# Optimization experiments

Measured on AMD Instinct MI355X. Metric: run time of the kernel, lower is better.

Reference implementation:

```python
import jax, jax.numpy as jnp
import numpy as np
import math

B, H, L = 8, 512, 4096
N2 = 32  # d_state // 2


def setup_inputs() -> dict:
    key = jax.random.key(0)
    ks = jax.random.split(key, 8)
    u = jax.random.normal(ks[0], (B, H, L), dtype=jnp.float32)
    C = jax.random.normal(ks[1], (H, N2, 2), dtype=jnp.float32)  # view_as_real of cfloat C
    # log_dt ~ Uniform[log(dt_min), log(dt_max)], dt_min=1e-3, dt_max=0.1
    log_dt = jax.random.uniform(ks[2], (H,), dtype=jnp.float32,
                                minval=math.log(0.001), maxval=math.log(0.1))
    log_A_real = jnp.log(0.5 * jnp.ones((H, N2), dtype=jnp.float32))
    A_imag = math.pi * jnp.broadcast_to(jnp.arange(N2, dtype=jnp.float32), (H, N2))
    D = jax.random.normal(ks[3], (H,), dtype=jnp.float32)
    # pointwise Conv1d(H, 2H, kernel_size=1): weight (2H, H), bias (2H)
    fan = 1.0 / math.sqrt(H)
    W = jax.random.uniform(ks[4], (2 * H, H), dtype=jnp.float32, minval=-fan, maxval=fan)
    b = jax.random.uniform(ks[5], (2 * H,), dtype=jnp.float32, minval=-fan, maxval=fan)
    return {"u": u, "C": C, "log_dt": log_dt, "log_A_real": log_A_real,
            "A_imag": A_imag, "D": D, "W": W, "b": b}


def reference(u, C, log_dt, log_A_real, A_imag, D, W, b):
    Lb = u.shape[-1]
    # --- S4DKernel: kernel k of shape (H, L) ---
    dt = jnp.exp(log_dt)                                  # (H,)
    Cc = C[..., 0] + 1j * C[..., 1]                       # (H, N2) complex
    A = -jnp.exp(log_A_real) + 1j * A_imag                # (H, N2)
    dtA = A * dt[:, None]                                 # (H, N2)
    # Vandermonde: exp(dtA * l) for l in [0, L)
    K = jnp.exp(dtA[:, :, None] * jnp.arange(Lb, dtype=jnp.float32))  # (H, N2, L)
    Cmod = Cc * (jnp.exp(dtA) - 1.0) / A                  # (H, N2)
    k = 2.0 * jnp.einsum('hn,hnl->hl', Cmod, K).real      # (H, L)
    # --- FFT convolution (length 2L, causal) ---
    n = 2 * Lb
    k_f = jnp.fft.rfft(k, n=n)                            # (H, L+1)
    u_f = jnp.fft.rfft(u, n=n)                            # (B, H, L+1)
    y = jnp.fft.irfft(u_f * k_f, n=n)[..., :Lb]           # (B, H, L)
    # skip connection
    y = y + u * D[:, None]
    # activation (torch nn.GELU default = exact erf form)
    y = jax.nn.gelu(y, approximate=False)
    # pointwise conv (H -> 2H) + GLU over channel dim
    y = jnp.einsum('oh,bhl->bol', W, y) + b[None, :, None]  # (B, 2H, L)
    a, g = jnp.split(y, 2, axis=1)
    return a * jax.nn.sigmoid(g)                          # (B, H, L)
```

## Files before the change

kernel.cpp:

```cpp
#include <hip/hip_runtime.h>
#include <hip/hip_bf16.h>

constexpr int Bn = 8, Hn = 512, Ln = 4096, N2n = 32;

typedef _Float16 f16;
typedef __attribute__((ext_vector_type(8))) _Float16 f16x8;
typedef __attribute__((ext_vector_type(4))) _Float16 f16x4;
typedef __attribute__((ext_vector_type(2))) _Float16 f16x2;
typedef __attribute__((ext_vector_type(4))) float f32x4;

typedef void __attribute__((address_space(1))) gvoid;
typedef void __attribute__((address_space(3))) lvoid;

__global__ __launch_bounds__(64) void k_mats1(
    const float* __restrict__ C, const float* __restrict__ log_dt,
    const float* __restrict__ logA, const float* __restrict__ Aim,
    f16* __restrict__ Vg, f16* __restrict__ A3g, float2* __restrict__ w64g) {
  __shared__ f16 VT[64 * 64];
  __shared__ f16 QT[64 * 64];
  __shared__ float kp[64][33];
  __shared__ float ks[64];
  const int h = blockIdx.x, tid = threadIdx.x, n = tid & 31;

  if (tid < 32) {
    const int idx = h * N2n + n;
    float dt = expf(log_dt[h]);
    float Ar = -expf(logA[idx]);
    float Ai = Aim[idx];
    float dr = Ar * dt, di = Ai * dt;
    float er = expf(dr);
    float wr = er * cosf(di), wi = er * sinf(di);
    float den = Ar * Ar + Ai * Ai;
    float e1r = wr - 1.0f, e1i = wi;
    float tr = (e1r * Ar + e1i * Ai) / den;
    float ti = (e1i * Ar - e1r * Ai) / den;
    float Cr = C[idx * 2 + 0], Ci = C[idx * 2 + 1];
    float c2r = 2.0f * (Cr * tr - Ci * ti);
    float c2i = 2.0f * (Cr * ti + Ci * tr);

    float wpr = 1.f, wpi = 0.f;
    for (int p = 0; p <= 64; ++p) {
      float cwr = c2r * wpr - c2i * wpi;
      float cwi = c2r * wpi + c2i * wpr;
      if (p < 64) {
        const int j = 63 - p, ch = j >> 3, jo = j & 7;
        const int s0 = 2 * n, s1 = 2 * n + 1;
        VT[s0 * 64 + ((ch ^ (s0 & 7)) * 8) + jo] = (f16)wpr;
        VT[s1 * 64 + ((ch ^ (s1 & 7)) * 8) + jo] = (f16)wpi;
        kp[p][n] = cwr;
      }
      if (p >= 1) {
        const int t = p - 1, c0 = 2 * n;
        const int ch = (c0 >> 3) ^ (t & 7);
        QT[t * 64 + ch * 8 + (c0 & 7)]     = (f16)cwr;
        QT[t * 64 + ch * 8 + (c0 & 7) + 1] = (f16)(-cwi);
      }
      if (p == 64) w64g[h * 32 + n] = make_float2(wpr, wpi);
      float nr = wpr * wr - wpi * wi;
      float ni = wpr * wi + wpi * wr;
      wpr = nr; wpi = ni;
    }
  }
  __syncthreads();
  float s = 0.f;
#pragma unroll
  for (int m = 0; m < 32; ++m) s += kp[tid][m];
  ks[tid] = s;
  __syncthreads();
  const int t = tid;
#pragma unroll
  for (int c = 0; c < 8; ++c) {
    f16x8 row;
#pragma unroll
    for (int jo = 0; jo < 8; ++jo) {
      int j = c * 8 + jo;
      row[jo] = (j <= t) ? (f16)ks[t - j] : (f16)0.f;
    }
    *(f16x8*)&A3g[(size_t)h * 8192 + t * 128 + ((c ^ (t & 7)) * 8)] = row;
  }
#pragma unroll
  for (int c = 0; c < 8; ++c)
    *(f16x8*)&Vg[(size_t)h * 4096 + tid * 64 + c * 8] = *(f16x8*)&VT[tid * 64 + c * 8];
#pragma unroll
  for (int c = 0; c < 8; ++c)
    *(f16x8*)&A3g[(size_t)h * 8192 + tid * 128 + 64 + c * 8] = *(f16x8*)&QT[tid * 64 + c * 8];
}

__global__ void conv_w(const float* __restrict__ W, f16* __restrict__ Wh) {
  int i = blockIdx.x * 256 + threadIdx.x;
  if (i < 2 * Hn * Hn) Wh[i] = (f16)W[i];
}

__global__ __launch_bounds__(256, 4) void s4d_mid(
    const float* __restrict__ u, const f16* __restrict__ Vg,
    const f16* __restrict__ A3g, const float2* __restrict__ w64g,
    const float* __restrict__ Dv, f16* __restrict__ yg) {
  __shared__ f16 MATS[8192];
  __shared__ f16 U[4096];
  __shared__ f16 LE[4096];
  __shared__ float2 Pbuf[4][32];
  const int tid = threadIdx.x, wid = tid >> 6, lane = tid & 63;
  const int h = ((blockIdx.x >> 6) << 3) | (blockIdx.x & 7);
  const int b = (blockIdx.x >> 3) & 7;
  const float Dh = Dv[h];

#pragma unroll
  for (int q = 0; q < 2; ++q)
    __builtin_amdgcn_global_load_lds((const gvoid*)(Vg + (size_t)h * 4096 + (q * 256 + tid) * 8),
                                     (lvoid*)&MATS[(q * 256 + wid * 64) * 8], 16, 0, 0);
#pragma unroll
  for (int i = 0; i < 4; ++i) {
    int e = (i * 256 + tid) * 4;
    float4 uv = *(const float4*)(u + ((size_t)(b * Hn + h)) * Ln + e);
    int col = e >> 6, j = e & 63;
    f16x4 hv = {(f16)uv.x, (f16)uv.y, (f16)uv.z, (f16)uv.w};
    *(f16x4*)&U[col * 64 + ((j >> 3) ^ (col & 7)) * 8 + (j & 7)] = hv;
  }
  asm volatile("s_waitcnt vmcnt(0)" ::: "memory");
  __syncthreads();

  const int col = wid * 16 + (lane & 15);
  f32x4 acc[4];
#pragma unroll
  for (int i = 0; i < 4; ++i) acc[i] = (f32x4){0.f, 0.f, 0.f, 0.f};
#pragma unroll
  for (int ks = 0; ks < 2; ++ks) {
    const int kc = ks * 4 + (lane >> 4);
    f16x8 bv = *(const f16x8*)&U[col * 64 + ((kc ^ (col & 7)) * 8)];
#pragma unroll
    for (int mf = 0; mf < 4; ++mf) {
      int row = mf * 16 + (lane & 15);
      f16x8 a = *(const f16x8*)&MATS[row * 64 + ((kc ^ (row & 7)) * 8)];
      acc[mf] = __builtin_amdgcn_mfma_f32_16x16x32_f16(a, bv, acc[mf], 0, 0, 0);
    }
  }
  __syncthreads();

#pragma unroll
  for (int q = 0; q < 4; ++q)
    __builtin_amdgcn_global_load_lds((const gvoid*)(A3g + (size_t)h * 8192 + (q * 256 + tid) * 8),
                                     (lvoid*)&MATS[(q * 256 + wid * 64) * 8], 16, 0, 0);

#pragma unroll
  for (int mf = 0; mf < 4; ++mf) {
    int st0 = mf * 16 + (lane >> 4) * 4;
    f16x4 o = {(f16)acc[mf][0], (f16)acc[mf][1], (f16)acc[mf][2], (f16)acc[mf][3]};
    *(f16x4*)&LE[col * 64 + (((st0 >> 3) ^ (col & 7)) << 3) + (st0 & 7)] = o;
  }
  __syncthreads();

  {
    const int n = lane & 31, q = wid;
    const float2 wT = w64g[h * 32 + n];
    float qr = wT.x, qi = wT.y;
#pragma unroll
    for (int s = 0; s < 4; ++s) {
      float nr = qr * qr - qi * qi;
      float ni = 2.f * qr * qi;
      qr = nr; qi = ni;
    }
    f16x2 Lb[16];
    float er = 0.f, ei = 0.f;
    if (lane < 32) {
#pragma unroll
      for (int k = 0; k < 16; ++k) {
        int blk = q * 16 + k;
        int fi = blk * 64 + (((n >> 2) ^ (blk & 7)) << 3) + ((n & 3) << 1);
        Lb[k] = *(const f16x2*)&LE[fi];
      }
#pragma unroll
      for (int k = 0; k < 16; ++k) {
        float nr = fmaf(wT.x, er, fmaf(-wT.y, ei, (float)Lb[k][0]));
        float ni = fmaf(wT.y, er, fmaf(wT.x, ei, (float)Lb[k][1]));
        er = nr; ei = ni;
      }
      Pbuf[q][n] = make_float2(er, ei);
    }
    __syncthreads();
    if (lane < 32) {
      float orr = 0.f, oii = 0.f;
      for (int p = 0; p < q; ++p) {
        float2 Pp = Pbuf[p][n];
        float nr = fmaf(qr, orr, fmaf(-qi, oii, Pp.x));
        float ni = fmaf(qi, orr, fmaf(qr, oii, Pp.y));
        orr = nr; oii = ni;
      }
      er = orr; ei = oii;
#pragma unroll
      for (int k = 0; k < 16; ++k) {
        int blk = q * 16 + k;
        int fi = blk * 64 + (((n >> 2) ^ (blk & 7)) << 3) + ((n & 3) << 1);
        *(f16x2*)&LE[fi] = (f16x2){(f16)er, (f16)ei};
        float nr = fmaf(wT.x, er, fmaf(-wT.y, ei, (float)Lb[k][0]));
        float ni = fmaf(wT.y, er, fmaf(wT.x, ei, (float)Lb[k][1]));
        er = nr; ei = ni;
      }
    }
  }
  asm volatile("s_waitcnt vmcnt(0)" ::: "memory");
  __syncthreads();

  f32x4 acc4[4];
#pragma unroll
  for (int i = 0; i < 4; ++i) acc4[i] = (f32x4){0.f, 0.f, 0.f, 0.f};
#pragma unroll
  for (int ks = 0; ks < 4; ++ks) {
    const int kc = ks * 4 + (lane >> 4);
    f16x8 bf;
    if (ks < 2) bf = *(const f16x8*)&U[col * 64 + ((kc ^ (col & 7)) << 3)];
    else        bf = *(const f16x8*)&LE[col * 64 + (((kc - 8) ^ (col & 7)) << 3)];
#pragma unroll
    for (int mf = 0; mf < 4; ++mf) {
      int row = mf * 16 + (lane & 15);
      f16x8 af = *(const f16x8*)&MATS[row * 128 + ((kc ^ (row & 7)) << 3)];
      acc4[mf] = __builtin_amdgcn_mfma_f32_16x16x32_f16(af, bf, acc4[mf], 0, 0, 0);
    }
  }
  const int t0 = (lane >> 4) * 4;
#pragma unroll
  for (int mf = 0; mf < 4; ++mf) {
    const int tb = mf * 16 + t0;
    f16x4 uq = *(const f16x4*)&U[col * 64 + (((tb >> 3) ^ (col & 7)) << 3) + (tb & 7)];
    f16x4 o;
#pragma unroll
    for (int r = 0; r < 4; ++r) {
      float v = acc4[mf][r] + Dh * (float)uq[r];
      float g2 = v * fmaf(0.0713548163f, v * v, 1.5957691216f);
      o[r] = (f16)(v * __builtin_amdgcn_rcpf(1.0f + __expf(-g2)));
    }
    *(f16x4*)&yg[((size_t)(b * Hn + h)) * Ln + col * 64 + tb] = o;
  }
}

__global__ __launch_bounds__(256) void k_transpose(
    const f16* __restrict__ yg, f16* __restrict__ gyT) {
  __shared__ float T[64][65];
  const int bid = blockIdx.x, tid = threadIdx.x;
  const int b = bid >> 9, hg = (bid >> 6) & 7, lg = bid & 63;
  const int h0 = hg * 64, l0 = lg * 64;
  const int hi = tid >> 2, lc = (tid & 3) * 16;
  const f16* src = yg + ((size_t)(b * Hn + h0 + hi)) * Ln + l0 + lc;
  f16x8 v0 = *(const f16x8*)src;
  f16x8 v1 = *(const f16x8*)(src + 8);
#pragma unroll
  for (int e = 0; e < 8; ++e) T[lc + e][hi] = (float)v0[e];
#pragma unroll
  for (int e = 0; e < 8; ++e) T[lc + 8 + e][hi] = (float)v1[e];
  __syncthreads();
  const int li = tid >> 2, hc = (tid & 3) * 16;
  f16x8 o0, o1;
#pragma unroll
  for (int e = 0; e < 8; ++e) o0[e] = (f16)T[li][hc + e];
#pragma unroll
  for (int e = 0; e < 8; ++e) o1[e] = (f16)T[li][hc + 8 + e];
  f16* dst = gyT + ((size_t)b * Ln + l0 + li) * Hn + h0 + hc;
  *(f16x8*)dst = o0;
  *(f16x8*)(dst + 8) = o1;
}

__global__ __launch_bounds__(256, 3) void s4d_gemm(
    const f16* __restrict__ Wh, const f16* __restrict__ gyT,
    const float* __restrict__ bias, float* __restrict__ out) {
  __shared__ f16 As[2][2][64][32];
  __shared__ f16 Bs[2][128][32];
  __shared__ float biasS[2][64];
  const int tid = threadIdx.x;
  const int wid = tid >> 6, lane = tid & 63;
  const int nt = blockIdx.x & 255;
  const int mt = blockIdx.x >> 8;
  const int b = nt >> 5;
  const int l0 = (nt & 31) * 128;
  const int m0 = mt * 64;
  const int isG = wid >> 1;
  const int wn = wid & 1;

  if (tid < 64) biasS[0][tid] = bias[m0 + tid];
  else if (tid < 128) biasS[1][tid - 64] = bias[Hn + m0 + (tid - 64)];

  const int srow = lane >> 2;
  const int sp = lane & 3;

#define S4(r) ((((r) & 3)) ^ (((r) >> 2) & 3))

#define STAGE(BUF, KT)                                                                    \
  {                                                                                       \
    const int k0 = (KT) * 32;                                                             \
    _Pragma("unroll")                                                                     \
    for (int q = 0; q < 2; ++q) {                                                         \
      const int g = wid * 2 + q;                                                \
      const int ag = g >> 2, rq = g & 3;                                                  \
      const int r = rq * 16 + srow;                                                       \
      const f16* srcA = Wh + ((size_t)(ag * Hn + m0 + r) * 512 + k0 + ((sp ^ S4(r)) * 8)); \
      __builtin_amdgcn_global_load_lds((const gvoid*)srcA,                                \
          (lvoid*)&As[BUF][ag][rq * 16][0], 16, 0, 0);                                    \
    }                                                                                     \
    _Pragma("unroll")                                                                     \
    for (int q = 0; q < 2; ++q) {                                                         \
      const int rb = wid * 2 + q;                                               \
      const int r = rb * 16 + srow;                                                       \
      const f16* srcB = gyT + (((size_t)b * Ln + l0 + r) * Hn + k0 + ((sp ^ S4(r)) * 8)); \
      __builtin_amdgcn_global_load_lds((const gvoid*)srcB,                                \
          (lvoid*)&Bs[BUF][rb * 16][0], 16, 0, 0);                                        \
    }                                                                                     \
  }

  f32x4 acc[4][4];
#pragma unroll
  for (int i = 0; i < 4; ++i)
#pragma unroll
    for (int j = 0; j < 4; ++j) acc[i][j] = (f32x4){0.f, 0.f, 0.f, 0.f};

  STAGE(0, 0);
  asm volatile("s_waitcnt vmcnt(0)" ::: "memory");
  __syncthreads();

  const int kc = lane >> 4;
  for (int t = 0; t < 16; ++t) {
    const int cur = t & 1;
    if (t < 15) STAGE(cur ^ 1, t + 1);
    f16x8 af[4], bf[4];
#pragma unroll
    for (int mf = 0; mf < 4; ++mf) {
      const int row = mf * 16 + (lane & 15);
      af[mf] = *(const f16x8*)&As[cur][isG][row][(kc ^ S4(row)) * 8];
    }
#pragma unroll
    for (int nf = 0; nf < 4; ++nf) {
      const int cl = wn * 64 + nf * 16 + (lane & 15);
      bf[nf] = *(const f16x8*)&Bs[cur][cl][(kc ^ S4(cl)) * 8];
    }
#pragma unroll
    for (int mf = 0; mf < 4; ++mf)
#pragma unroll
      for (int nf = 0; nf < 4; ++nf)
        acc[mf][nf] = __builtin_amdgcn_mfma_f32_16x16x32_f16(af[mf], bf[nf], acc[mf][nf], 0, 0, 0);
    __syncthreads();
  }

  f16 (*SIG)[64][64] = (f16(*)[64][64]) & Bs[0][0][0];
  const int r0 = (lane >> 4) * 4, c0 = lane & 15;
  if (isG) {
#pragma unroll
    for (int mf = 0; mf < 4; ++mf) {
#pragma unroll
      for (int nf = 0; nf < 4; ++nf) {
#pragma unroll
        for (int r = 0; r < 4; ++r) {
          const int row = mf * 16 + r0 + r;
          float gv = acc[mf][nf][r] + biasS[1][row];
          SIG[wn][row][nf * 16 + c0] = (f16)__builtin_amdgcn_rcpf(1.0f + __expf(-gv));
        }
      }
    }
  }
  __syncthreads();
  if (!isG) {
#pragma unroll
    for (int mf = 0; mf < 4; ++mf) {
#pragma unroll
      for (int nf = 0; nf < 4; ++nf) {
#pragma unroll
        for (int r = 0; r < 4; ++r) {
          const int row = mf * 16 + r0 + r;
          const int col = nf * 16 + c0;
          float av = acc[mf][nf][r] + biasS[0][row];
          float sg = (float)SIG[wn][row][col];
          out[((size_t)b * Hn + m0 + row) * Ln + l0 + wn * 64 + col] = av * sg;
        }
      }
    }
  }
#undef STAGE
#undef S4
}

extern "C" void kernel_launch(void* const* d_in, const int* in_sizes, int n_in,
                              void* d_out, int out_size, void* d_ws, size_t ws_size,
                              hipStream_t stream) {
  (void)in_sizes; (void)n_in; (void)out_size; (void)ws_size;
  const float* u     = (const float*)d_in[0];
  const float* C     = (const float*)d_in[1];
  const float* logdt = (const float*)d_in[2];
  const float* logA  = (const float*)d_in[3];
  const float* Aim   = (const float*)d_in[4];
  const float* Dv    = (const float*)d_in[5];
  const float* W     = (const float*)d_in[6];
  const float* bias  = (const float*)d_in[7];
  float* out = (float*)d_out;

  char* ws = (char*)d_ws;
  f16*    gyT  = (f16*)ws;
  f16*    Vg   = (f16*)(ws + (size_t)(32 << 20));
  f16*    A3g  = (f16*)(ws + (size_t)(36 << 20));
  float2* w64g = (float2*)(ws + (size_t)(44 << 20));
  f16*    Wh   = (f16*)(ws + (size_t)(45 << 20));
  f16*    yg   = (f16*)d_out;

  hipLaunchKernelGGL(k_mats1, dim3(Hn), dim3(64), 0, stream, C, logdt, logA, Aim, Vg, A3g, w64g);
  hipLaunchKernelGGL(conv_w, dim3(2048), dim3(256), 0, stream, W, Wh);
  hipLaunchKernelGGL(s4d_mid, dim3(Hn * Bn), dim3(256), 0, stream, u, Vg, A3g, w64g, Dv, yg);
  hipLaunchKernelGGL(k_transpose, dim3(Bn * 8 * 64), dim3(256), 0, stream, yg, gyT);
  hipLaunchKernelGGL(s4d_gemm, dim3(8 * 256), dim3(256), 0, stream, Wh, gyT, bias, out);
}
```

Measured before the change: 107.7 us.

## Double K-tile depth in GLU GEMM with prefetch-two pipeline and 8-way swizzle

The GEMM K-step grows from 32 to 64, so the main loop runs 8 iterations with two MFMA sub-steps each instead of 16. Two stages are prefetched up front, and partial vmcnt waits with raw s_barrier let one tile's loads overlap compute on the other. The LDS swizzle changes to a 3-bit XOR to match the wider rows. The aim is fewer barriers and better hiding of global-to-LDS latency, at the cost of doubled LDS use and lower occupancy (launch bounds drop from 3 to 2 blocks).

```diff
diff --git a/kernel.cpp b/kernel.cpp
--- a/kernel.cpp
+++ b/kernel.cpp
@@ -258,11 +258,11 @@
   *(f16x8*)(dst + 8) = o1;
 }
 
-__global__ __launch_bounds__(256, 3) void s4d_gemm(
+__global__ __launch_bounds__(256, 2) void s4d_gemm(
     const f16* __restrict__ Wh, const f16* __restrict__ gyT,
     const float* __restrict__ bias, float* __restrict__ out) {
-  __shared__ f16 As[2][2][64][32];
-  __shared__ f16 Bs[2][128][32];
+  __shared__ f16 As[2][2][64][64];
+  __shared__ f16 Bs[2][128][64];
   __shared__ float biasS[2][64];
   const int tid = threadIdx.x;
   const int wid = tid >> 6, lane = tid & 63;
@@ -277,31 +277,24 @@
   if (tid < 64) biasS[0][tid] = bias[m0 + tid];
   else if (tid < 128) biasS[1][tid - 64] = bias[Hn + m0 + (tid - 64)];
 
-  const int srow = lane >> 2;
-  const int sp = lane & 3;
-
-#define S4(r) ((((r) & 3)) ^ (((r) >> 2) & 3))
+  const int srow = lane >> 3;
+  const int sks = ((lane & 7) ^ srow) * 8;
 
 #define STAGE(BUF, KT)                                                                    \
   {                                                                                       \
-    const int k0 = (KT) * 32;                                                             \
+    const int k0 = (KT) * 64;                                                             \
     _Pragma("unroll")                                                                     \
-    for (int q = 0; q < 2; ++q) {                                                         \
-      const int g = wid * 2 + q;                                                \
-      const int ag = g >> 2, rq = g & 3;                                                  \
-      const int r = rq * 16 + srow;                                                       \
-      const f16* srcA = Wh + ((size_t)(ag * Hn + m0 + r) * 512 + k0 + ((sp ^ S4(r)) * 8)); \
+    for (int q = 0; q < 4; ++q) {                                                         \
+      const int ga = q * 4 + wid;                                              \
+      const int role = ga >> 3, r0a = (ga & 7) * 8;                                       \
+      const f16* srcA = Wh + ((size_t)(role * Hn + m0 + r0a + srow) * 512 + k0 + sks);    \
       __builtin_amdgcn_global_load_lds((const gvoid*)srcA,                                \
-          (lvoid*)&As[BUF][ag][rq * 16][0], 16, 0, 0);                                    \
+          (lvoid*)&As[BUF][role][r0a][0], 16, 0, 0);                                      \
+      const int rb = ga * 8;                                                  \
+      const f16* srcB = gyT + (((size_t)b * Ln + l0 + rb + srow) * Hn + k0 + sks);        \
+      __builtin_amdgcn_global_load_lds((const gvoid*)srcB,                                \
+          (lvoid*)&Bs[BUF][rb][0], 16, 0, 0);                                             \
     }                                                                                     \
-    _Pragma("unroll")                                                                     \
-    for (int q = 0; q < 2; ++q) {                                                         \
-      const int rb = wid * 2 + q;                                               \
-      const int r = rb * 16 + srow;                                                       \
-      const f16* srcB = gyT + (((size_t)b * Ln + l0 + r) * Hn + k0 + ((sp ^ S4(r)) * 8)); \
-      __builtin_amdgcn_global_load_lds((const gvoid*)srcB,                                \
-          (lvoid*)&Bs[BUF][rb * 16][0], 16, 0, 0);                                        \
-    }                                                                                     \
   }
 
   f32x4 acc[4][4];
@@ -311,42 +304,51 @@
     for (int j = 0; j < 4; ++j) acc[i][j] = (f32x4){0.f, 0.f, 0.f, 0.f};
 
   STAGE(0, 0);
-  asm volatile("s_waitcnt vmcnt(0)" ::: "memory");
-  __syncthreads();
-
-  const int kc = lane >> 4;
-  for (int t = 0; t < 16; ++t) {
+  STAGE(1, 1);
+
+#pragma unroll
+  for (int t = 0; t < 8; ++t) {
     const int cur = t & 1;
-    if (t < 15) STAGE(cur ^ 1, t + 1);
-    f16x8 af[4], bf[4];
+    if (t < 7) { asm volatile("s_waitcnt vmcnt(8)" ::: "memory"); }
+    else       { asm volatile("s_waitcnt vmcnt(0)" ::: "memory"); }
+    __builtin_amdgcn_s_barrier();
+    __builtin_amdgcn_sched_barrier(0);
+#pragma unroll
+    for (int kk = 0; kk < 2; ++kk) {
+      const int kc = kk * 4 + (lane >> 4);
+      f16x8 af[4], bf[4];
+#pragma unroll
+      for (int mf = 0; mf < 4; ++mf) {
+        const int row = mf * 16 + (lane & 15);
+        af[mf] = *(const f16x8*)&As[cur][isG][row][(kc ^ (row & 7)) * 8];
+      }
+#pragma unroll
+      for (int nf = 0; nf < 4; ++nf) {
+        const int cl = wn * 64 + nf * 16 + (lane & 15);
+        bf[nf] = *(const f16x8*)&Bs[cur][cl][(kc ^ (cl & 7)) * 8];
+      }
+#pragma unroll
+      for (int mf = 0; mf < 4; ++mf)
+#pragma unroll
+        for (int nf = 0; nf < 4; ++nf)
+          acc[mf][nf] = __builtin_amdgcn_mfma_f32_16x16x32_f16(af[mf], bf[nf], acc[mf][nf], 0, 0, 0);
+    }
+    __builtin_amdgcn_sched_barrier(0);
+    __builtin_amdgcn_s_barrier();
+    if (t < 6) STAGE(cur, t + 2);
+  }
+
+  __syncthreads();
+  f16 (*SIG)[64][64] = (f16(*)[64][64]) & Bs[0][0][0];
+  const int r0e = (lane >> 4) * 4, c0 = lane & 15;
+  if (isG) {
 #pragma unroll
     for (int mf = 0; mf < 4; ++mf) {
-      const int row = mf * 16 + (lane & 15);
-      af[mf] = *(const f16x8*)&As[cur][isG][row][(kc ^ S4(row)) * 8];
-    }
-#pragma unroll
-    for (int nf = 0; nf < 4; ++nf) {
-      const int cl = wn * 64 + nf * 16 + (lane & 15);
-      bf[nf] = *(const f16x8*)&Bs[cur][cl][(kc ^ S4(cl)) * 8];
-    }
-#pragma unroll
-    for (int mf = 0; mf < 4; ++mf)
-#pragma unroll
-      for (int nf = 0; nf < 4; ++nf)
-        acc[mf][nf] = __builtin_amdgcn_mfma_f32_16x16x32_f16(af[mf], bf[nf], acc[mf][nf], 0, 0, 0);
-    __syncthreads();
-  }
-
-  f16 (*SIG)[64][64] = (f16(*)[64][64]) & Bs[0][0][0];
-  const int r0 = (lane >> 4) * 4, c0 = lane & 15;
-  if (isG) {
-#pragma unroll
-    for (int mf = 0; mf < 4; ++mf) {
 #pragma unroll
       for (int nf = 0; nf < 4; ++nf) {
 #pragma unroll
         for (int r = 0; r < 4; ++r) {
-          const int row = mf * 16 + r0 + r;
+          const int row = mf * 16 + r0e + r;
           float gv = acc[mf][nf][r] + biasS[1][row];
           SIG[wn][row][nf * 16 + c0] = (f16)__builtin_amdgcn_rcpf(1.0f + __expf(-gv));
         }
@@ -361,17 +363,16 @@
       for (int nf = 0; nf < 4; ++nf) {
 #pragma unroll
         for (int r = 0; r < 4; ++r) {
-          const int row = mf * 16 + r0 + r;
-          const int col = nf * 16 + c0;
+          const int row = mf * 16 + r0e + r;
+          const int colc = nf * 16 + c0;
           float av = acc[mf][nf][r] + biasS[0][row];
-          float sg = (float)SIG[wn][row][col];
-          out[((size_t)b * Hn + m0 + row) * Ln + l0 + wn * 64 + col] = av * sg;
+          float sg = (float)SIG[wn][row][colc];
+          out[((size_t)b * Hn + m0 + row) * Ln + l0 + wn * 64 + colc] = av * sg;
         }
       }
     }
   }
 #undef STAGE
-#undef S4
 }
 
 extern "C" void kernel_launch(void* const* d_in, const int* in_sizes, int n_in,
```

Result: slower. 112.9 us (+4.8%).
